# Kernel tuning notes

Hardware: AMD Instinct MI355X
Metric: run time of the kernel (lower is better)

The kernel has to match this reference:

```python
import jax, jax.numpy as jnp
import numpy as np


def setup_inputs() -> dict:
    key = jax.random.key(0)
    kx, kw = jax.random.split(key)
    B, IN, OUT = 8192, 4096, 4096
    x = jax.random.normal(kx, (B, IN), dtype=jnp.float32)
    # matches torch init: (rand*2-1)*0.001 -> uniform in [-0.001, 0.001]
    weight = jax.random.uniform(kw, (OUT, IN), dtype=jnp.float32, minval=-1.0, maxval=1.0) * 0.001
    return {"x": x, "weight": weight}


def reference(x, weight):
    # scaling factor = mean(|W|), detached
    scale = jax.lax.stop_gradient(jnp.mean(jnp.abs(weight)))
    binary_no_grad = scale * jnp.sign(weight)
    clipped = jnp.clip(weight, -1.0, 1.0)
    # straight-through estimator: fwd value = scale*sign(W), bwd grad = d(clip)/dW
    binary_weights = jax.lax.stop_gradient(binary_no_grad - clipped) + clipped
    # F.linear: y = x @ W^T  -> [B, OUT]
    return jnp.einsum('bi,oi->bo', x, binary_weights)
```

## Files before the change

kernel.cpp:

```cpp
#include <hip/hip_runtime.h>
#include <hip/hip_bf16.h>
#include <stdint.h>

typedef __attribute__((ext_vector_type(4))) int i32x4;

#define GLOAD(g, l) __builtin_amdgcn_global_load_lds(                      \
    (const __attribute__((address_space(1))) void*)(g),                    \
    (__attribute__((address_space(3))) void*)(l), 16, 0, 0)

#define MFMAI8 __builtin_amdgcn_mfma_i32_16x16x64_i8
#define BARRIER __builtin_amdgcn_s_barrier
#define LGKM0 asm volatile("s_waitcnt lgkmcnt(0)" ::: "memory")

__global__ __launch_bounds__(256) void wsign_kernel(
    const float* __restrict__ W, char* __restrict__ S,
    float* __restrict__ partials) {
  const int tid = threadIdx.x;
  const int base = blockIdx.x * 1024;
  const float4* wp = reinterpret_cast<const float4*>(W);
  int* sp = reinterpret_cast<int*>(S);
  float s = 0.f;
#pragma unroll
  for (int i = 0; i < 4; ++i) {
    const int idx = base + tid + 256 * i;
    float4 w = wp[idx];
    int b0 = (w.x > 0.f) - (w.x < 0.f);
    int b1 = (w.y > 0.f) - (w.y < 0.f);
    int b2 = (w.z > 0.f) - (w.z < 0.f);
    int b3 = (w.w > 0.f) - (w.w < 0.f);
    sp[idx] = (b0 & 255) | ((b1 & 255) << 8) | ((b2 & 255) << 16) |
              ((b3 & 255) << 24);
    s += fabsf(w.x) + fabsf(w.y) + fabsf(w.z) + fabsf(w.w);
  }
#pragma unroll
  for (int off = 32; off > 0; off >>= 1) s += __shfl_down(s, off, 64);
  __shared__ float sm[4];
  if ((tid & 63) == 0) sm[tid >> 6] = s;
  __syncthreads();
  if (tid == 0) partials[blockIdx.x] = sm[0] + sm[1] + sm[2] + sm[3];
}

__global__ __launch_bounds__(256) void xquant_kernel(
    const float* __restrict__ X, char* __restrict__ XQ,
    float* __restrict__ qrow) {
  const int row = blockIdx.x;
  const int tid = threadIdx.x;
  const float4* xr = reinterpret_cast<const float4*>(X + (size_t)row * 4096);
  int* xo = reinterpret_cast<int*>(XQ + (size_t)row * 4096);
  float4 v[4];
  float am = 0.f;
#pragma unroll
  for (int i = 0; i < 4; ++i) {
    v[i] = xr[tid + 256 * i];
    am = fmaxf(am, fmaxf(fmaxf(fabsf(v[i].x), fabsf(v[i].y)),
                         fmaxf(fabsf(v[i].z), fabsf(v[i].w))));
  }
#pragma unroll
  for (int off = 1; off < 64; off <<= 1)
    am = fmaxf(am, __shfl_xor(am, off, 64));
  __shared__ float wm[4];
  if ((tid & 63) == 0) wm[tid >> 6] = am;
  __syncthreads();
  float amax = fmaxf(fmaxf(wm[0], wm[1]), fmaxf(wm[2], wm[3]));
  amax = fmaxf(amax, 1e-20f);
  const float rq = 127.f / amax;
#pragma unroll
  for (int i = 0; i < 4; ++i) {
    int b0 = __float2int_rn(v[i].x * rq);
    int b1 = __float2int_rn(v[i].y * rq);
    int b2 = __float2int_rn(v[i].z * rq);
    int b3 = __float2int_rn(v[i].w * rq);
    xo[tid + 256 * i] = (b0 & 255) | ((b1 & 255) << 8) | ((b2 & 255) << 16) |
                        ((b3 & 255) << 24);
  }
  if (tid == 0) qrow[row] = amax * (1.f / 127.f);
}

__global__ __launch_bounds__(256) void finalize_kernel(
    const float* __restrict__ partials, float* __restrict__ scale) {
  const int tid = threadIdx.x;
  float s = 0.f;
  for (int i = tid; i < 4096; i += 256) s += partials[i];
#pragma unroll
  for (int off = 32; off > 0; off >>= 1) s += __shfl_down(s, off, 64);
  __shared__ float sm[4];
  if ((tid & 63) == 0) sm[tid >> 6] = s;
  __syncthreads();
  if (tid == 0) scale[0] = (sm[0] + sm[1] + sm[2] + sm[3]) * (1.0f / 16777216.0f);
}

__global__ __launch_bounds__(512, 2) void gemm_i8_kernel(
    const char* __restrict__ A,
    const char* __restrict__ B,
    const float* __restrict__ scale_p, const float* __restrict__ qrow,
    float* __restrict__ C) {
  constexpr int M = 8192, N = 4096, K = 4096;
  constexpr int NT = K / 128;
  constexpr int NI = NT / 2;
  __shared__ __align__(16) char lds[131072];

  const int tid = threadIdx.x;
  const int wid = tid >> 6;
  const int lane = tid & 63;
  const int wr = wid >> 2;
  const int wc = wid & 3;
  const int bh = wc >> 1;
  const int bsub = (wc & 1) * 8192;
  const int fr = lane & 15;
  const int fq = lane >> 4;
  const int sk0 = ((fq) ^ (fr & 7)) * 16;
  const int sk1 = ((4 + fq) ^ (fr & 7)) * 16;

  const int bid = blockIdx.x;
  const int swz = (bid & 7) * 64 + (bid >> 3);
  const int tm = swz >> 4, tn = swz & 15;

  const int srow = tid >> 3;
  const int sg = (tid & 7) ^ (srow & 7);
  const char* aSrc0 = A + (size_t)(tm * 256 + srow) * K + sg * 16;
  const char* aSrc1 = aSrc0 + (size_t)128 * K;
  const char* bSrc0 = B + (size_t)(tn * 256 + srow) * K + sg * 16;
  const char* bSrc1 = bSrc0 + (size_t)128 * K;

#define STAGE(srcBase, slotIdx, koff)                              \
  do {                                                             \
    const char* _s = (srcBase) + (koff);                           \
    char* _d = lds + (slotIdx) * 16384 + wid * 1024;               \
    GLOAD(_s, _d);                                                 \
    GLOAD(_s + (size_t)64 * K, _d + 8192);                         \
  } while (0)

  const char* aSp0 = lds + (0 + wr) * 16384 + fr * 128;
  const char* aSp1 = lds + (2 + wr) * 16384 + fr * 128;
  const char* bSp0 = lds + (4 + bh) * 16384 + bsub + fr * 128;
  const char* bSp1 = lds + (6 + bh) * 16384 + bsub + fr * 128;

  i32x4 acc[8][4];
#pragma unroll
  for (int m = 0; m < 8; ++m)
#pragma unroll
    for (int n = 0; n < 4; ++n) acc[m][n] = (i32x4){0, 0, 0, 0};

#define RD_B(bS)                                                       \
  _Pragma("unroll") for (int n = 0; n < 4; ++n) {                      \
    bq[n][0] = *(const i32x4*)((bS) + n * 2048 + sk0);                 \
    bq[n][1] = *(const i32x4*)((bS) + n * 2048 + sk1);                 \
  }
#define RD_A(aS, q)                                                    \
  _Pragma("unroll") for (int m2 = 0; m2 < 2; ++m2) {                   \
    av[m2][0] = *(const i32x4*)((aS) + (2 * (q) + m2) * 2048 + sk0);   \
    av[m2][1] = *(const i32x4*)((aS) + (2 * (q) + m2) * 2048 + sk1);   \
  }
#define QMFMA(q)                                                       \
  do {                                                                 \
    __builtin_amdgcn_s_setprio(1);                                     \
    _Pragma("unroll") for (int m2 = 0; m2 < 2; ++m2)                   \
        _Pragma("unroll") for (int n = 0; n < 4; ++n) {                \
      acc[2 * (q) + m2][n] =                                           \
          MFMAI8(av[m2][0], bq[n][0], acc[2 * (q) + m2][n], 0, 0, 0);  \
      acc[2 * (q) + m2][n] =                                           \
          MFMAI8(av[m2][1], bq[n][1], acc[2 * (q) + m2][n], 0, 0, 0);  \
    }                                                                  \
    __builtin_amdgcn_s_setprio(0);                                     \
  } while (0)

  STAGE(bSrc0, 4, 0);
  STAGE(bSrc1, 5, 0);
  STAGE(aSrc0, 0, 0);
  STAGE(aSrc1, 1, 0);
  STAGE(bSrc0, 6, 128);
  STAGE(bSrc1, 7, 128);
  asm volatile("s_waitcnt vmcnt(4)" ::: "memory");
  BARRIER();

  for (int i = 0; i < NI; ++i) {
    const int t0 = 2 * i;
    const int k1 = (t0 + 1) * 128, k2 = (t0 + 2) * 128, k3 = (t0 + 3) * 128;
    i32x4 bq[4][2], av[2][2];

    RD_B(bSp0);
    RD_A(aSp0, 0);
    STAGE(aSrc0, 2, k1);
    LGKM0; BARRIER(); QMFMA(0);

    RD_A(aSp0, 1);
    STAGE(aSrc1, 3, k1);
    LGKM0; BARRIER(); QMFMA(1);

    RD_A(aSp0, 2);
    if (t0 + 2 < NT) STAGE(bSrc0, 4, k2);
    LGKM0; BARRIER(); QMFMA(2);

    RD_A(aSp0, 3);
    if (t0 + 2 < NT) {
      STAGE(bSrc1, 5, k2);
      asm volatile("s_waitcnt vmcnt(4)" ::: "memory");
    } else {
      asm volatile("s_waitcnt vmcnt(0)" ::: "memory");
    }
    LGKM0; BARRIER(); QMFMA(3);

    RD_B(bSp1);
    RD_A(aSp1, 0);
    if (t0 + 2 < NT) STAGE(aSrc0, 0, k2);
    LGKM0; BARRIER(); QMFMA(0);

    RD_A(aSp1, 1);
    if (t0 + 2 < NT) STAGE(aSrc1, 1, k2);
    LGKM0; BARRIER(); QMFMA(1);

    RD_A(aSp1, 2);
    if (t0 + 3 < NT) STAGE(bSrc0, 6, k3);
    LGKM0; BARRIER(); QMFMA(2);

    RD_A(aSp1, 3);
    if (t0 + 3 < NT) {
      STAGE(bSrc1, 7, k3);
      asm volatile("s_waitcnt vmcnt(4)" ::: "memory");
    }
    LGKM0; BARRIER(); QMFMA(3);
  }

  const float sc = *scale_p;
  const int crow0 = tm * 256 + wr * 128 + fq * 4;
  const int ccol0 = tn * 256 + wc * 64 + fr;
#pragma unroll
  for (int m = 0; m < 8; ++m) {
    const int row = crow0 + m * 16;
    float q[4];
#pragma unroll
    for (int j = 0; j < 4; ++j) q[j] = sc * qrow[row + j];
#pragma unroll
    for (int n = 0; n < 4; ++n) {
      i32x4 v = acc[m][n];
      float* cp = C + (size_t)row * N + ccol0 + n * 16;
#pragma unroll
      for (int j = 0; j < 4; ++j) cp[(size_t)j * N] = (float)v[j] * q[j];
    }
  }
#undef STAGE
#undef RD_A
#undef RD_B
#undef QMFMA
}

extern "C" void kernel_launch(void* const* d_in, const int* in_sizes, int n_in,
                              void* d_out, int out_size, void* d_ws,
                              size_t ws_size, hipStream_t stream) {
  const float* x = (const float*)d_in[0];
  const float* w = (const float*)d_in[1];
  float* out = (float*)d_out;

  char* ws = (char*)d_ws;
  char* xq = ws;
  char* sq = ws + 33554432;
  float* qrow = (float*)(ws + 50331648);
  float* partials = (float*)(ws + 50331648 + 32768);
  float* scale = (float*)(ws + 50331648 + 32768 + 16384);

  wsign_kernel<<<4096, 256, 0, stream>>>(w, sq, partials);
  xquant_kernel<<<8192, 256, 0, stream>>>(x, xq, qrow);
  finalize_kernel<<<1, 256, 0, stream>>>(partials, scale);
  gemm_i8_kernel<<<512, 512, 0, stream>>>(xq, sq, scale, qrow, out);
}
```

Measured before the change: 176.3 us.

## Double-buffer A fragment registers and prefetch LDS reads ahead of MFMA

```diff
diff --git a/kernel.cpp b/kernel.cpp
--- a/kernel.cpp
+++ b/kernel.cpp
@@ -10,7 +10,6 @@
 
 #define MFMAI8 __builtin_amdgcn_mfma_i32_16x16x64_i8
 #define BARRIER __builtin_amdgcn_s_barrier
-#define LGKM0 asm volatile("s_waitcnt lgkmcnt(0)" ::: "memory")
 
 __global__ __launch_bounds__(256) void wsign_kernel(
     const float* __restrict__ W, char* __restrict__ S,
@@ -146,12 +145,12 @@
     bq[n][0] = *(const i32x4*)((bS) + n * 2048 + sk0);                 \
     bq[n][1] = *(const i32x4*)((bS) + n * 2048 + sk1);                 \
   }
-#define RD_A(aS, q)                                                    \
+#define RD_A(dst, aS, q)                                               \
   _Pragma("unroll") for (int m2 = 0; m2 < 2; ++m2) {                   \
-    av[m2][0] = *(const i32x4*)((aS) + (2 * (q) + m2) * 2048 + sk0);   \
-    av[m2][1] = *(const i32x4*)((aS) + (2 * (q) + m2) * 2048 + sk1);   \
-  }
-#define QMFMA(q)                                                       \
+    dst[m2][0] = *(const i32x4*)((aS) + (2 * (q) + m2) * 2048 + sk0);  \
+    dst[m2][1] = *(const i32x4*)((aS) + (2 * (q) + m2) * 2048 + sk1);  \
+  }
+#define QMFMA(av, q)                                                   \
   do {                                                                 \
     __builtin_amdgcn_s_setprio(1);                                     \
     _Pragma("unroll") for (int m2 = 0; m2 < 2; ++m2)                   \
@@ -169,56 +168,68 @@
   STAGE(aSrc0, 0, 0);
   STAGE(aSrc1, 1, 0);
   STAGE(bSrc0, 6, 128);
-  STAGE(bSrc1, 7, 128);
-  asm volatile("s_waitcnt vmcnt(4)" ::: "memory");
+  asm volatile("s_waitcnt vmcnt(2)" ::: "memory");
   BARRIER();
+
+  i32x4 bq[4][2], av0[2][2], av1[2][2];
+  RD_B(bSp0);
+  RD_A(av0, aSp0, 0);
 
   for (int i = 0; i < NI; ++i) {
     const int t0 = 2 * i;
     const int k1 = (t0 + 1) * 128, k2 = (t0 + 2) * 128, k3 = (t0 + 3) * 128;
-    i32x4 bq[4][2], av[2][2];
-
-    RD_B(bSp0);
-    RD_A(aSp0, 0);
+
+    RD_A(av1, aSp0, 1);
+    STAGE(bSrc1, 7, k1);
+    BARRIER();
+    QMFMA(av0, 0);
+
+    RD_A(av0, aSp0, 2);
     STAGE(aSrc0, 2, k1);
-    LGKM0; BARRIER(); QMFMA(0);
-
-    RD_A(aSp0, 1);
+    BARRIER();
+    QMFMA(av1, 1);
+
+    RD_A(av1, aSp0, 3);
     STAGE(aSrc1, 3, k1);
-    LGKM0; BARRIER(); QMFMA(1);
-
-    RD_A(aSp0, 2);
-    if (t0 + 2 < NT) STAGE(bSrc0, 4, k2);
-    LGKM0; BARRIER(); QMFMA(2);
-
-    RD_A(aSp0, 3);
+    BARRIER();
+    QMFMA(av0, 2);
+
     if (t0 + 2 < NT) {
-      STAGE(bSrc1, 5, k2);
-      asm volatile("s_waitcnt vmcnt(4)" ::: "memory");
+      STAGE(bSrc0, 4, k2);
+      asm volatile("s_waitcnt vmcnt(2)" ::: "memory");
     } else {
       asm volatile("s_waitcnt vmcnt(0)" ::: "memory");
     }
-    LGKM0; BARRIER(); QMFMA(3);
-
+    BARRIER();
+    QMFMA(av1, 3);
     RD_B(bSp1);
-    RD_A(aSp1, 0);
+    RD_A(av0, aSp1, 0);
+
+    RD_A(av1, aSp1, 1);
+    if (t0 + 2 < NT) STAGE(bSrc1, 5, k2);
+    BARRIER();
+    QMFMA(av0, 0);
+
+    RD_A(av0, aSp1, 2);
     if (t0 + 2 < NT) STAGE(aSrc0, 0, k2);
-    LGKM0; BARRIER(); QMFMA(0);
-
-    RD_A(aSp1, 1);
+    BARRIER();
+    QMFMA(av1, 1);
+
+    RD_A(av1, aSp1, 3);
     if (t0 + 2 < NT) STAGE(aSrc1, 1, k2);
-    LGKM0; BARRIER(); QMFMA(1);
-
-    RD_A(aSp1, 2);
-    if (t0 + 3 < NT) STAGE(bSrc0, 6, k3);
-    LGKM0; BARRIER(); QMFMA(2);
-
-    RD_A(aSp1, 3);
-    if (t0 + 3 < NT) {
-      STAGE(bSrc1, 7, k3);
-      asm volatile("s_waitcnt vmcnt(4)" ::: "memory");
-    }
-    LGKM0; BARRIER(); QMFMA(3);
+    BARRIER();
+    QMFMA(av0, 2);
+
+    if (t0 + 2 < NT) {
+      STAGE(bSrc0, 6, k3);
+      asm volatile("s_waitcnt vmcnt(2)" ::: "memory");
+    }
+    BARRIER();
+    QMFMA(av1, 3);
+    if (t0 + 2 < NT) {
+      RD_B(bSp0);
+      RD_A(av0, aSp0, 0);
+    }
   }
 
   const float sc = *scale_p;
```

Measured after the change: 174.8 us. About the same (-0.8%).
